# Kernel tuning notes

Measured on AMD Instinct MI355X. Metric: run time of the kernel, lower is better.

## Reference

```python
import jax, jax.numpy as jnp
import numpy as np

N_NODES = 100000

def gcn_conv(x, W, b, row, col, n):
    # PyG GCNConv: linear transform, then D^-1/2 A_hat D^-1/2 aggregation (+bias).
    xw = x @ W                                            # [N, out]
    deg = jax.ops.segment_sum(jnp.ones_like(col, dtype=xw.dtype), col, num_segments=n)
    dinv = jnp.where(deg > 0, jax.lax.rsqrt(jnp.maximum(deg, 1e-12)), 0.0)
    norm = dinv[row] * dinv[col]                          # [E]
    msgs = xw[row] * norm[:, None]                        # gather + scale
    out = jax.ops.segment_sum(msgs, col, num_segments=n)  # scatter-add
    return out + b


def setup_inputs() -> dict:
    key = jax.random.key(0)
    k = jax.random.split(key, 9)
    n, e = N_NODES, 1600000
    d_in, d_h, d_out = 128, 64, 40
    def glorot(kk, fi, fo):
        s = jnp.sqrt(6.0 / (fi + fo))
        return jax.random.uniform(kk, (fi, fo), jnp.float32, -s, s)
    return {
        "x": jax.random.normal(k[0], (n, d_in), jnp.float32),
        "edge_index": jax.random.randint(k[1], (2, e), 0, n, jnp.int64),
        "W1": glorot(k[2], d_in, d_h), "b1": jnp.zeros((d_h,), jnp.float32),
        "W2": glorot(k[3], d_h, d_h),  "b2": jnp.zeros((d_h,), jnp.float32),
        "W3": glorot(k[4], d_h, d_out), "b3": jnp.zeros((d_out,), jnp.float32),
    }


def reference(x, edge_index, W1, b1, W2, b2, W3, b3):
    n = x.shape[0]
    loops = jnp.arange(n, dtype=edge_index.dtype)
    row = jnp.concatenate([edge_index[0], loops])  # self-loops added, as in GCNConv
    col = jnp.concatenate([edge_index[1], loops])
    h = jax.nn.relu(gcn_conv(x, W1, b1, row, col, n))
    h = jax.nn.relu(gcn_conv(h, W2, b2, row, col, n))
    return gcn_conv(h, W3, b3, row, col, n)
```

## Files before the change

kernel.cpp:

```cpp
#include <hip/hip_runtime.h>
#include <hip/hip_fp16.h>

constexpr int TPB = 256;
constexpr int SH = 9;
constexpr int BD = 1 << SH;
constexpr int CHUNK = 4096;

typedef _Float16 half8 __attribute__((ext_vector_type(8)));
typedef float float4v __attribute__((ext_vector_type(4)));

__device__ __forceinline__ int wave_incl_scan(int x, int lane) {
#pragma unroll
  for (int d = 1; d < 64; d <<= 1) {
    int y = __shfl_up(x, d);
    if (lane >= d) x += y;
  }
  return x;
}


__global__ void bin_kernel(const int* __restrict__ row, const int* __restrict__ col,
                           int* __restrict__ bcur, int2* __restrict__ binned,
                           int e, int nb, int cap) {
  __shared__ int h[512];
  __shared__ int base[512];
  for (int i = threadIdx.x; i < nb; i += TPB) h[i] = 0;
  __syncthreads();
  int cb = blockIdx.x * CHUNK;
  int lim = min(cb + CHUNK, e);
  for (int i = cb + threadIdx.x; i < lim; i += TPB)
    atomicAdd(&h[col[i] >> SH], 1);
  __syncthreads();
  for (int i = threadIdx.x; i < nb; i += TPB) {
    int c = h[i];
    base[i] = c ? (i * cap + atomicAdd(&bcur[i], c)) : 0;
    h[i] = 0;
  }
  __syncthreads();
  for (int i = cb + threadIdx.x; i < lim; i += TPB) {
    int c = col[i];
    int b = c >> SH;
    int p = base[b] + atomicAdd(&h[b], 1);
    binned[p] = make_int2(row[i], c);
  }
}

__global__ __launch_bounds__(512) void count_place_kernel(
    const int2* __restrict__ binned, const int* __restrict__ bcnt, int cap,
    int2* __restrict__ offs2, float* __restrict__ dinv, int* __restrict__ csr, int n) {
  __shared__ int cnt[BD];
  __shared__ int wsum[8];
  int t = threadIdx.x, lane = t & 63, wv = t >> 6;
  int b = blockIdx.x;
  int c0 = b << SH;
  int ndst = min(BD, n - c0);
  cnt[t] = 0;
  __syncthreads();
  int beg = b * cap;
  int end = beg + bcnt[b];
  for (int i = beg + t; i < end; i += 512)
    atomicAdd(&cnt[binned[i].y - c0], 1);
  __syncthreads();
  int v = cnt[t];
  int ps = wave_incl_scan(v, lane);
  if (lane == 63) wsum[wv] = ps;
  __syncthreads();
  int woff = 0;
#pragma unroll
  for (int w = 0; w < 8; w++) woff += (w < wv) ? wsum[w] : 0;
  int ex = woff + ps - v;
  if (t < ndst) {
    offs2[c0 + t] = make_int2(beg + ex, beg + ex + v);
    dinv[c0 + t] = rsqrtf(1.0f + (float)v);
  }
  __syncthreads();
  cnt[t] = beg + ex;
  __syncthreads();
  for (int i = beg + t; i < end; i += 512) {
    int2 rc = binned[i];
    int p = atomicAdd(&cnt[rc.y - c0], 1);
    csr[p] = rc.x;
  }
}


template <int K, int M, int CT, int KT>
__device__ __forceinline__ void pack_one(const float* __restrict__ W,
                                         _Float16* __restrict__ P, int idx) {
  if (idx >= CT * KT * 64 * 8) return;
  int j = idx & 7;
  int lane = (idx >> 3) & 63;
  int f = idx >> 9;
  int kt = f % KT, ct = f / KT;
  int c = ct * 16 + (lane & 15);
  int k = kt * 32 + (lane >> 4) * 8 + j;
  float v = (c < M) ? W[k * M + c] : 0.f;
  P[idx] = (_Float16)v;
}

__global__ __launch_bounds__(256) void pack_all_kernel(
    const float* __restrict__ W1, const float* __restrict__ W2,
    const float* __restrict__ W3, _Float16* __restrict__ P1,
    _Float16* __restrict__ P2, _Float16* __restrict__ P3, int* __restrict__ bcur) {
  int blk = blockIdx.x, t = threadIdx.x;
  if (blk < 32) {
    pack_one<128, 64, 4, 4>(W1, P1, blk * 256 + t);
  } else if (blk < 48) {
    pack_one<64, 64, 4, 2>(W2, P2, (blk - 32) * 256 + t);
  } else if (blk < 60) {
    pack_one<64, 40, 3, 2>(W3, P3, (blk - 48) * 256 + t);
  } else {
    bcur[t] = 0;
    bcur[t + 256] = 0;
  }
}


template <int K, int M, int CT>
__global__ __launch_bounds__(256) void gemm_mfma_f32in(const float* __restrict__ x,
                                                       const _Float16* __restrict__ PW,
                                                       const float* __restrict__ dinv,
                                                       _Float16* __restrict__ out, int n) {
  constexpr int KT = K / 32;
  int lane = threadIdx.x & 63, wv = threadIdx.x >> 6;
  int m = lane & 15, q = lane >> 4;
  int row0w = blockIdx.x * 64 + wv * 16;
  int arow = row0w + m;
  int ar = arow < n ? arow : n - 1;
  const half8* pw = (const half8*)PW;

  float4v acc[CT];
#pragma unroll
  for (int ct = 0; ct < CT; ct++) acc[ct] = (float4v){0.f, 0.f, 0.f, 0.f};

#pragma unroll
  for (int kt = 0; kt < KT; kt++) {
    const float* xp = x + (size_t)ar * K + kt * 32 + q * 8;
    float4 x0 = *(const float4*)xp;
    float4 x1 = *(const float4*)(xp + 4);
    half8 a;
    a[0] = (_Float16)x0.x; a[1] = (_Float16)x0.y;
    a[2] = (_Float16)x0.z; a[3] = (_Float16)x0.w;
    a[4] = (_Float16)x1.x; a[5] = (_Float16)x1.y;
    a[6] = (_Float16)x1.z; a[7] = (_Float16)x1.w;
#pragma unroll
    for (int ct = 0; ct < CT; ct++) {
      half8 b = pw[(ct * KT + kt) * 64 + lane];
      acc[ct] = __builtin_amdgcn_mfma_f32_16x16x32_f16(a, b, acc[ct], 0, 0, 0);
    }
  }
  int r0 = row0w + q * 4;
  float dv[4];
#pragma unroll
  for (int reg = 0; reg < 4; reg++) dv[reg] = (r0 + reg < n) ? dinv[r0 + reg] : 0.f;
#pragma unroll
  for (int ct = 0; ct < CT; ct++) {
    int c = ct * 16 + m;
    if (c < M) {
#pragma unroll
      for (int reg = 0; reg < 4; reg++) {
        int r = r0 + reg;
        if (r < n) out[(size_t)r * M + c] = (_Float16)(acc[ct][reg] * dv[reg]);
      }
    }
  }
}

template <int K, int M, int CT>
__global__ __launch_bounds__(256) void gemm_mfma_f16in(const _Float16* __restrict__ x,
                                                       const _Float16* __restrict__ PW,
                                                       const float* __restrict__ dinv,
                                                       _Float16* __restrict__ out, int n) {
  constexpr int KT = K / 32;
  int lane = threadIdx.x & 63, wv = threadIdx.x >> 6;
  int m = lane & 15, q = lane >> 4;
  int row0w = blockIdx.x * 64 + wv * 16;
  int arow = row0w + m;
  int ar = arow < n ? arow : n - 1;
  const half8* pw = (const half8*)PW;

  float4v acc[CT];
#pragma unroll
  for (int ct = 0; ct < CT; ct++) acc[ct] = (float4v){0.f, 0.f, 0.f, 0.f};

#pragma unroll
  for (int kt = 0; kt < KT; kt++) {
    half8 a = *(const half8*)(x + (size_t)ar * K + kt * 32 + q * 8);
#pragma unroll
    for (int ct = 0; ct < CT; ct++) {
      half8 b = pw[(ct * KT + kt) * 64 + lane];
      acc[ct] = __builtin_amdgcn_mfma_f32_16x16x32_f16(a, b, acc[ct], 0, 0, 0);
    }
  }
  int r0 = row0w + q * 4;
  float dv[4];
#pragma unroll
  for (int reg = 0; reg < 4; reg++) dv[reg] = (r0 + reg < n) ? dinv[r0 + reg] : 0.f;
#pragma unroll
  for (int ct = 0; ct < CT; ct++) {
    int c = ct * 16 + m;
    if (c < M) {
#pragma unroll
      for (int reg = 0; reg < 4; reg++) {
        int r = r0 + reg;
        if (r < n) out[(size_t)r * M + c] = (_Float16)(acc[ct][reg] * dv[reg]);
      }
    }
  }
}

template <int K, int M, int CT>
__global__ __launch_bounds__(256) void gemm_mfma_f16in_f32out(
    const _Float16* __restrict__ x, const _Float16* __restrict__ PW,
    const float* __restrict__ bias, float* __restrict__ out, int n) {
  constexpr int KT = K / 32;
  int lane = threadIdx.x & 63, wv = threadIdx.x >> 6;
  int m = lane & 15, q = lane >> 4;
  int row0w = blockIdx.x * 64 + wv * 16;
  int arow = row0w + m;
  int ar = arow < n ? arow : n - 1;
  const half8* pw = (const half8*)PW;

  float4v acc[CT];
#pragma unroll
  for (int ct = 0; ct < CT; ct++) acc[ct] = (float4v){0.f, 0.f, 0.f, 0.f};

#pragma unroll
  for (int kt = 0; kt < KT; kt++) {
    half8 a = *(const half8*)(x + (size_t)ar * K + kt * 32 + q * 8);
#pragma unroll
    for (int ct = 0; ct < CT; ct++) {
      half8 b = pw[(ct * KT + kt) * 64 + lane];
      acc[ct] = __builtin_amdgcn_mfma_f32_16x16x32_f16(a, b, acc[ct], 0, 0, 0);
    }
  }
  int r0 = row0w + q * 4;
#pragma unroll
  for (int ct = 0; ct < CT; ct++) {
    int c = ct * 16 + m;
    if (c < M) {
      float bb = bias[c];
#pragma unroll
      for (int reg = 0; reg < 4; reg++) {
        int r = r0 + reg;
        if (r < n) out[(size_t)r * M + c] = acc[ct][reg] + bb;
      }
    }
  }
}


__device__ __forceinline__ void h8_add(uint4 u, float* acc) {
  __half2 h0 = *(__half2*)&u.x, h1 = *(__half2*)&u.y;
  __half2 h2 = *(__half2*)&u.z, h3 = *(__half2*)&u.w;
  float2 f0 = __half22float2(h0), f1 = __half22float2(h1);
  float2 f2 = __half22float2(h2), f3 = __half22float2(h3);
  acc[0] += f0.x; acc[1] += f0.y; acc[2] += f1.x; acc[3] += f1.y;
  acc[4] += f2.x; acc[5] += f2.y; acc[6] += f3.x; acc[7] += f3.y;
}

template <int MODE>
__global__ __launch_bounds__(256) void agg_kernel(
    const uint4* __restrict__ xw4, const float* __restrict__ dinv,
    const int* __restrict__ csr, const int2* __restrict__ offs2,
    const float* __restrict__ bias, uint4* __restrict__ out4, int n) {
  int lane = threadIdx.x & 63, wv = threadIdx.x >> 6;
  int slot = lane >> 3, fl = lane & 7;
  int sb = slot << 3;
  int i = blockIdx.x * 32 + wv * 8 + slot;
  bool valid = i < n;
  int ic = valid ? i : n - 1;
  int2 oe = offs2[ic];
  int beg = oe.x;
  int end = valid ? oe.y : beg;
  float di = dinv[ic];
  float acc[8] = {0.f, 0.f, 0.f, 0.f, 0.f, 0.f, 0.f, 0.f};
  h8_add(xw4[(size_t)ic * 8 + fl], acc);

  for (int b = beg; b < end; b += 8) {
    int idx = b + fl;
    int rr = 0;
    if (idx < end) rr = csr[idx];
    int cnt = end - b;
    uint4 u[8];
#pragma unroll
    for (int j = 0; j < 8; j++) {
      if (j < cnt) {
        int r = __shfl(rr, sb + j);
        u[j] = xw4[(size_t)r * 8 + fl];
      }
    }
#pragma unroll
    for (int j = 0; j < 8; j++) {
      if (j < cnt) h8_add(u[j], acc);
    }
  }

  if (valid) {
    float o[8];
    if (MODE < 2) {
      const float4* b4 = (const float4*)bias;
      float4 ba = b4[fl * 2], bb = b4[fl * 2 + 1];
      o[0] = fmaxf(acc[0] * di + ba.x, 0.f);
      o[1] = fmaxf(acc[1] * di + ba.y, 0.f);
      o[2] = fmaxf(acc[2] * di + ba.z, 0.f);
      o[3] = fmaxf(acc[3] * di + ba.w, 0.f);
      o[4] = fmaxf(acc[4] * di + bb.x, 0.f);
      o[5] = fmaxf(acc[5] * di + bb.y, 0.f);
      o[6] = fmaxf(acc[6] * di + bb.z, 0.f);
      o[7] = fmaxf(acc[7] * di + bb.w, 0.f);
      if (MODE == 1) {
#pragma unroll
        for (int k = 0; k < 8; k++) o[k] *= di;
      }
    } else {
#pragma unroll
      for (int k = 0; k < 8; k++) o[k] = acc[k] * di;
    }
    __half2 h0 = __float22half2_rn(make_float2(o[0], o[1]));
    __half2 h1 = __float22half2_rn(make_float2(o[2], o[3]));
    __half2 h2 = __float22half2_rn(make_float2(o[4], o[5]));
    __half2 h3 = __float22half2_rn(make_float2(o[6], o[7]));
    uint4 u;
    u.x = *(unsigned*)&h0;
    u.y = *(unsigned*)&h1;
    u.z = *(unsigned*)&h2;
    u.w = *(unsigned*)&h3;
    out4[(size_t)i * 8 + fl] = u;
  }
}


extern "C" void kernel_launch(void* const* d_in, const int* in_sizes, int n_in,
                              void* d_out, int out_size, void* d_ws, size_t ws_size,
                              hipStream_t stream) {
  const float* x  = (const float*)d_in[0];
  const int*   ei = (const int*)d_in[1];
  const float* W1 = (const float*)d_in[2];
  const float* b1 = (const float*)d_in[3];
  const float* W2 = (const float*)d_in[4];
  const float* b2 = (const float*)d_in[5];
  const float* W3 = (const float*)d_in[6];
  const float* b3 = (const float*)d_in[7];

  int n = in_sizes[0] / 128;
  int e = in_sizes[1] / 2;
  const int* rowA = ei;
  const int* colA = ei + e;

  int nb = (n + BD - 1) >> SH;
  int meanb = e / nb;
  int cap = meanb + (meanb / 4 > 1024 ? meanb / 4 : 1024);
  int nch = (e + CHUNK - 1) / CHUNK;

  size_t off = 0;
  auto alloc = [&](size_t bytes) {
    void* p = (char*)d_ws + off;
    off += (bytes + 255) & ~(size_t)255;
    return p;
  };
  __half* bufA  = (__half*)alloc((size_t)n * 64 * 4);
  __half* bufB  = (__half*)alloc((size_t)n * 64 * 4);
  int2*  offs2  = (int2*)alloc((size_t)n * 8);
  float* dinv   = (float*)alloc((size_t)n * 4);
  int*   csr    = (int*)alloc((size_t)nb * cap * 4);
  int*   bcur   = (int*)alloc(512 * 4);
  _Float16* PW1 = (_Float16*)alloc(4 * 4 * 64 * 8 * 2);
  _Float16* PW2 = (_Float16*)alloc(4 * 2 * 64 * 8 * 2);
  _Float16* PW3 = (_Float16*)alloc(3 * 2 * 64 * 8 * 2);
  int2*  binned = (int2*)bufA;
  (void)ws_size; (void)n_in; (void)out_size;

  pack_all_kernel<<<61, TPB, 0, stream>>>(W1, W2, W3, PW1, PW2, PW3, bcur);
  bin_kernel<<<nch, TPB, 0, stream>>>(rowA, colA, bcur, binned, e, nb, cap);
  count_place_kernel<<<nb, 512, 0, stream>>>(binned, bcur, cap, offs2, dinv, csr, n);

  int gmf = (n + 63) / 64;
  int gagg = (n + 31) / 32;
  gemm_mfma_f32in<128, 64, 4><<<gmf, TPB, 0, stream>>>(x, PW1, dinv, (_Float16*)bufA, n);
  agg_kernel<0><<<gagg, TPB, 0, stream>>>((const uint4*)bufA, dinv, csr, offs2,
                                          b1, (uint4*)bufB, n);
  gemm_mfma_f16in<64, 64, 4><<<gmf, TPB, 0, stream>>>((const _Float16*)bufB, PW2, dinv,
                                                      (_Float16*)bufA, n);
  agg_kernel<1><<<gagg, TPB, 0, stream>>>((const uint4*)bufA, dinv, csr, offs2,
                                          b2, (uint4*)bufB, n);
  agg_kernel<2><<<gagg, TPB, 0, stream>>>((const uint4*)bufB, dinv, csr, offs2,
                                          nullptr, (uint4*)bufA, n);
  gemm_mfma_f16in_f32out<64, 40, 3><<<gmf, TPB, 0, stream>>>((const _Float16*)bufA, PW3,
                                                             b3, (float*)d_out, n);
}
```

Measured before the change: 281.2 us.

## Fuse aggregation with following GEMM via LDS tile and widen per-node lanes

The first and third aggregations are merged with the GEMM that follows them. Each block aggregates 64 nodes into an fp16 LDS tile, then runs MFMA on that tile, which avoids writing the intermediate activations to global memory and reading them back. Aggregation now gives each node 16 lanes: two halves split the neighbours and are combined with a shuffle, and the next batch of CSR indices is prefetched. The cost is fewer nodes in flight per wave in the fused kernels (a serial loop over 4 nodes per slot), which may hurt latency hiding on the gather.

Result: faster. 256.5 us (-8.8%).

```diff
diff --git a/kernel.cpp b/kernel.cpp
--- a/kernel.cpp
+++ b/kernel.cpp
@@ -166,89 +166,6 @@
   }
 }
 
-template <int K, int M, int CT>
-__global__ __launch_bounds__(256) void gemm_mfma_f16in(const _Float16* __restrict__ x,
-                                                       const _Float16* __restrict__ PW,
-                                                       const float* __restrict__ dinv,
-                                                       _Float16* __restrict__ out, int n) {
-  constexpr int KT = K / 32;
-  int lane = threadIdx.x & 63, wv = threadIdx.x >> 6;
-  int m = lane & 15, q = lane >> 4;
-  int row0w = blockIdx.x * 64 + wv * 16;
-  int arow = row0w + m;
-  int ar = arow < n ? arow : n - 1;
-  const half8* pw = (const half8*)PW;
-
-  float4v acc[CT];
-#pragma unroll
-  for (int ct = 0; ct < CT; ct++) acc[ct] = (float4v){0.f, 0.f, 0.f, 0.f};
-
-#pragma unroll
-  for (int kt = 0; kt < KT; kt++) {
-    half8 a = *(const half8*)(x + (size_t)ar * K + kt * 32 + q * 8);
-#pragma unroll
-    for (int ct = 0; ct < CT; ct++) {
-      half8 b = pw[(ct * KT + kt) * 64 + lane];
-      acc[ct] = __builtin_amdgcn_mfma_f32_16x16x32_f16(a, b, acc[ct], 0, 0, 0);
-    }
-  }
-  int r0 = row0w + q * 4;
-  float dv[4];
-#pragma unroll
-  for (int reg = 0; reg < 4; reg++) dv[reg] = (r0 + reg < n) ? dinv[r0 + reg] : 0.f;
-#pragma unroll
-  for (int ct = 0; ct < CT; ct++) {
-    int c = ct * 16 + m;
-    if (c < M) {
-#pragma unroll
-      for (int reg = 0; reg < 4; reg++) {
-        int r = r0 + reg;
-        if (r < n) out[(size_t)r * M + c] = (_Float16)(acc[ct][reg] * dv[reg]);
-      }
-    }
-  }
-}
-
-template <int K, int M, int CT>
-__global__ __launch_bounds__(256) void gemm_mfma_f16in_f32out(
-    const _Float16* __restrict__ x, const _Float16* __restrict__ PW,
-    const float* __restrict__ bias, float* __restrict__ out, int n) {
-  constexpr int KT = K / 32;
-  int lane = threadIdx.x & 63, wv = threadIdx.x >> 6;
-  int m = lane & 15, q = lane >> 4;
-  int row0w = blockIdx.x * 64 + wv * 16;
-  int arow = row0w + m;
-  int ar = arow < n ? arow : n - 1;
-  const half8* pw = (const half8*)PW;
-
-  float4v acc[CT];
-#pragma unroll
-  for (int ct = 0; ct < CT; ct++) acc[ct] = (float4v){0.f, 0.f, 0.f, 0.f};
-
-#pragma unroll
-  for (int kt = 0; kt < KT; kt++) {
-    half8 a = *(const half8*)(x + (size_t)ar * K + kt * 32 + q * 8);
-#pragma unroll
-    for (int ct = 0; ct < CT; ct++) {
-      half8 b = pw[(ct * KT + kt) * 64 + lane];
-      acc[ct] = __builtin_amdgcn_mfma_f32_16x16x32_f16(a, b, acc[ct], 0, 0, 0);
-    }
-  }
-  int r0 = row0w + q * 4;
-#pragma unroll
-  for (int ct = 0; ct < CT; ct++) {
-    int c = ct * 16 + m;
-    if (c < M) {
-      float bb = bias[c];
-#pragma unroll
-      for (int reg = 0; reg < 4; reg++) {
-        int r = r0 + reg;
-        if (r < n) out[(size_t)r * M + c] = acc[ct][reg] + bb;
-      }
-    }
-  }
-}
-
 
 __device__ __forceinline__ void h8_add(uint4 u, float* acc) {
   __half2 h0 = *(__half2*)&u.x, h1 = *(__half2*)&u.y;
@@ -259,15 +176,62 @@
   acc[4] += f2.x; acc[5] += f2.y; acc[6] += f3.x; acc[7] += f3.y;
 }
 
-template <int MODE>
-__global__ __launch_bounds__(256) void agg_kernel(
+__device__ __forceinline__ uint4 pack_h8(const float* o) {
+  __half2 h0 = __float22half2_rn(make_float2(o[0], o[1]));
+  __half2 h1 = __float22half2_rn(make_float2(o[2], o[3]));
+  __half2 h2 = __float22half2_rn(make_float2(o[4], o[5]));
+  __half2 h3 = __float22half2_rn(make_float2(o[6], o[7]));
+  uint4 u;
+  u.x = *(unsigned*)&h0;
+  u.y = *(unsigned*)&h1;
+  u.z = *(unsigned*)&h2;
+  u.w = *(unsigned*)&h3;
+  return u;
+}
+
+__device__ __forceinline__ void agg_node(const uint4* __restrict__ xw4,
+                                         const int* __restrict__ csr,
+                                         int beg, int end, int sb, int half,
+                                         int fl, int fl16, float* acc) {
+  int b = beg;
+  int idx0 = b + fl16;
+  int rr = (idx0 < end) ? csr[idx0] : 0;
+  while (b < end) {
+    int bn = b + 16;
+    int idxn = bn + fl16;
+    int rn = (idxn < end) ? csr[idxn] : 0;
+    int cnt = end - b;
+    uint4 u[8];
+    int r[8];
+#pragma unroll
+    for (int j = 0; j < 8; j++) {
+      int ej = 2 * j + half;
+      r[j] = __shfl(rr, sb + ej);
+    }
+#pragma unroll
+    for (int j = 0; j < 8; j++) {
+      int ej = 2 * j + half;
+      if (ej < cnt) u[j] = xw4[(size_t)r[j] * 8 + fl];
+    }
+#pragma unroll
+    for (int j = 0; j < 8; j++) {
+      int ej = 2 * j + half;
+      if (ej < cnt) h8_add(u[j], acc);
+    }
+    rr = rn;
+    b = bn;
+  }
+}
+
+
+__global__ __launch_bounds__(256) void agg_mid_kernel(
     const uint4* __restrict__ xw4, const float* __restrict__ dinv,
     const int* __restrict__ csr, const int2* __restrict__ offs2,
     const float* __restrict__ bias, uint4* __restrict__ out4, int n) {
   int lane = threadIdx.x & 63, wv = threadIdx.x >> 6;
-  int slot = lane >> 3, fl = lane & 7;
-  int sb = slot << 3;
-  int i = blockIdx.x * 32 + wv * 8 + slot;
+  int sl = lane >> 4, fl16 = lane & 15, half = fl16 >> 3, fl = fl16 & 7;
+  int sb = sl << 4;
+  int i = blockIdx.x * 16 + wv * 4 + sl;
   bool valid = i < n;
   int ic = valid ? i : n - 1;
   int2 oe = offs2[ic];
@@ -275,31 +239,61 @@
   int end = valid ? oe.y : beg;
   float di = dinv[ic];
   float acc[8] = {0.f, 0.f, 0.f, 0.f, 0.f, 0.f, 0.f, 0.f};
-  h8_add(xw4[(size_t)ic * 8 + fl], acc);
-
-  for (int b = beg; b < end; b += 8) {
-    int idx = b + fl;
-    int rr = 0;
-    if (idx < end) rr = csr[idx];
-    int cnt = end - b;
-    uint4 u[8];
-#pragma unroll
-    for (int j = 0; j < 8; j++) {
-      if (j < cnt) {
-        int r = __shfl(rr, sb + j);
-        u[j] = xw4[(size_t)r * 8 + fl];
-      }
-    }
-#pragma unroll
-    for (int j = 0; j < 8; j++) {
-      if (j < cnt) h8_add(u[j], acc);
-    }
-  }
-
-  if (valid) {
+  if (!half) h8_add(xw4[(size_t)ic * 8 + fl], acc);
+  agg_node(xw4, csr, beg, end, sb, half, fl, fl16, acc);
+#pragma unroll
+  for (int k = 0; k < 8; k++) acc[k] += __shfl_xor(acc[k], 8);
+
+  if (valid && !half) {
+    const float4* b4 = (const float4*)bias;
+    float4 ba = b4[fl * 2], bb = b4[fl * 2 + 1];
     float o[8];
-    if (MODE < 2) {
-      const float4* b4 = (const float4*)bias;
+    o[0] = fmaxf(acc[0] * di + ba.x, 0.f) * di;
+    o[1] = fmaxf(acc[1] * di + ba.y, 0.f) * di;
+    o[2] = fmaxf(acc[2] * di + ba.z, 0.f) * di;
+    o[3] = fmaxf(acc[3] * di + ba.w, 0.f) * di;
+    o[4] = fmaxf(acc[4] * di + bb.x, 0.f) * di;
+    o[5] = fmaxf(acc[5] * di + bb.y, 0.f) * di;
+    o[6] = fmaxf(acc[6] * di + bb.z, 0.f) * di;
+    o[7] = fmaxf(acc[7] * di + bb.w, 0.f) * di;
+    out4[(size_t)i * 8 + fl] = pack_h8(o);
+  }
+}
+
+
+template <int M, int CT, int FMODE>
+__global__ __launch_bounds__(256) void fused_agg_gemm(
+    const uint4* __restrict__ xw4, const float* __restrict__ dinv,
+    const int* __restrict__ csr, const int2* __restrict__ offs2,
+    const float* __restrict__ biasA, const float* __restrict__ biasG,
+    const _Float16* __restrict__ PW, void* __restrict__ outp, int n) {
+  constexpr int KT = 2;
+  __shared__ _Float16 tile[64 * 72];
+  int lane = threadIdx.x & 63, wv = threadIdx.x >> 6;
+  int sl = lane >> 4, fl16 = lane & 15, half = fl16 >> 3, fl = fl16 & 7;
+  int sb = sl << 4;
+  int slot_id = wv * 4 + sl;
+  int base = blockIdx.x * 64;
+
+#pragma unroll 1
+  for (int nd = 0; nd < 4; nd++) {
+    int l = slot_id * 4 + nd;
+    int i = base + l;
+    bool valid = i < n;
+    int ic = valid ? i : n - 1;
+    int2 oe = offs2[ic];
+    int beg = oe.x;
+    int end = valid ? oe.y : beg;
+    float di = dinv[ic];
+    float acc[8] = {0.f, 0.f, 0.f, 0.f, 0.f, 0.f, 0.f, 0.f};
+    if (!half) h8_add(xw4[(size_t)ic * 8 + fl], acc);
+    agg_node(xw4, csr, beg, end, sb, half, fl, fl16, acc);
+#pragma unroll
+    for (int k = 0; k < 8; k++) acc[k] += __shfl_xor(acc[k], 8);
+
+    float o[8];
+    if (FMODE == 0) {
+      const float4* b4 = (const float4*)biasA;
       float4 ba = b4[fl * 2], bb = b4[fl * 2 + 1];
       o[0] = fmaxf(acc[0] * di + ba.x, 0.f);
       o[1] = fmaxf(acc[1] * di + ba.y, 0.f);
@@ -309,24 +303,60 @@
       o[5] = fmaxf(acc[5] * di + bb.y, 0.f);
       o[6] = fmaxf(acc[6] * di + bb.z, 0.f);
       o[7] = fmaxf(acc[7] * di + bb.w, 0.f);
-      if (MODE == 1) {
-#pragma unroll
-        for (int k = 0; k < 8; k++) o[k] *= di;
+    } else {
+#pragma unroll
+      for (int k = 0; k < 8; k++) o[k] = acc[k] * di;
+    }
+    if (!half) *(uint4*)&tile[(size_t)l * 72 + fl * 8] = pack_h8(o);
+  }
+  __syncthreads();
+
+  int m = lane & 15, q = lane >> 4;
+  int lrow = wv * 16 + m;
+  const half8* pw = (const half8*)PW;
+  float4v accd[CT];
+#pragma unroll
+  for (int ct = 0; ct < CT; ct++) accd[ct] = (float4v){0.f, 0.f, 0.f, 0.f};
+#pragma unroll
+  for (int kt = 0; kt < KT; kt++) {
+    half8 a = *(const half8*)&tile[lrow * 72 + kt * 32 + q * 8];
+#pragma unroll
+    for (int ct = 0; ct < CT; ct++) {
+      half8 b = pw[(ct * KT + kt) * 64 + lane];
+      accd[ct] = __builtin_amdgcn_mfma_f32_16x16x32_f16(a, b, accd[ct], 0, 0, 0);
+    }
+  }
+  int r0 = base + wv * 16 + q * 4;
+  if (FMODE == 0) {
+    _Float16* out = (_Float16*)outp;
+    float dv[4];
+#pragma unroll
+    for (int reg = 0; reg < 4; reg++) dv[reg] = (r0 + reg < n) ? dinv[r0 + reg] : 0.f;
+#pragma unroll
+    for (int ct = 0; ct < CT; ct++) {
+      int c = ct * 16 + m;
+      if (c < M) {
+#pragma unroll
+        for (int reg = 0; reg < 4; reg++) {
+          int r = r0 + reg;
+          if (r < n) out[(size_t)r * M + c] = (_Float16)(accd[ct][reg] * dv[reg]);
+        }
       }
-    } else {
-#pragma unroll
-      for (int k = 0; k < 8; k++) o[k] = acc[k] * di;
-    }
-    __half2 h0 = __float22half2_rn(make_float2(o[0], o[1]));
-    __half2 h1 = __float22half2_rn(make_float2(o[2], o[3]));
-    __half2 h2 = __float22half2_rn(make_float2(o[4], o[5]));
-    __half2 h3 = __float22half2_rn(make_float2(o[6], o[7]));
-    uint4 u;
-    u.x = *(unsigned*)&h0;
-    u.y = *(unsigned*)&h1;
-    u.z = *(unsigned*)&h2;
-    u.w = *(unsigned*)&h3;
-    out4[(size_t)i * 8 + fl] = u;
+    }
+  } else {
+    float* out = (float*)outp;
+#pragma unroll
+    for (int ct = 0; ct < CT; ct++) {
+      int c = ct * 16 + m;
+      if (c < M) {
+        float bb = biasG[c];
+#pragma unroll
+        for (int reg = 0; reg < 4; reg++) {
+          int r = r0 + reg;
+          if (r < n) out[(size_t)r * M + c] = accd[ct][reg] + bb;
+        }
+      }
+    }
   }
 }
 
@@ -376,16 +406,13 @@
   count_place_kernel<<<nb, 512, 0, stream>>>(binned, bcur, cap, offs2, dinv, csr, n);
 
   int gmf = (n + 63) / 64;
-  int gagg = (n + 31) / 32;
+  int gagg = (n + 15) / 16;
+
   gemm_mfma_f32in<128, 64, 4><<<gmf, TPB, 0, stream>>>(x, PW1, dinv, (_Float16*)bufA, n);
-  agg_kernel<0><<<gagg, TPB, 0, stream>>>((const uint4*)bufA, dinv, csr, offs2,
-                                          b1, (uint4*)bufB, n);
-  gemm_mfma_f16in<64, 64, 4><<<gmf, TPB, 0, stream>>>((const _Float16*)bufB, PW2, dinv,
-                                                      (_Float16*)bufA, n);
-  agg_kernel<1><<<gagg, TPB, 0, stream>>>((const uint4*)bufA, dinv, csr, offs2,
-                                          b2, (uint4*)bufB, n);
-  agg_kernel<2><<<gagg, TPB, 0, stream>>>((const uint4*)bufB, dinv, csr, offs2,
-                                          nullptr, (uint4*)bufA, n);
-  gemm_mfma_f16in_f32out<64, 40, 3><<<gmf, TPB, 0, stream>>>((const _Float16*)bufA, PW3,
-                                                             b3, (float*)d_out, n);
-}
+  fused_agg_gemm<64, 4, 0><<<gmf, TPB, 0, stream>>>(
+      (const uint4*)bufA, dinv, csr, offs2, b1, nullptr, PW2, bufB, n);
+  agg_mid_kernel<<<gagg, TPB, 0, stream>>>((const uint4*)bufB, dinv, csr, offs2,
+                                           b2, (uint4*)bufA, n);
+  fused_agg_gemm<40, 3, 1><<<gmf, TPB, 0, stream>>>(
+      (const uint4*)bufA, dinv, csr, offs2, nullptr, b3, PW3, d_out, n);
+}
```

## Pack binned edges into 32-bit words and prefetch CSR indices in aggregation

Applied to the files above, without the earlier changes.

Binning now packs the local destination offset (9 bits) and the source row (23 bits) into a single int, which halves the binned-edge traffic in bin and count_place. The aggregation kernel drops the shuffle-based index broadcast. Each 8-lane group now loads 16 neighbor indices directly per iteration and prefetches the next 16 while it gathers features, aiming for more memory-level parallelism. The costs are a 2^23 node limit on row ids and more registers. Every lane also reads the same csr entries redundantly.

Result: slower. 312.2 us (+11.1%).

```diff
diff --git a/kernel.cpp b/kernel.cpp
--- a/kernel.cpp
+++ b/kernel.cpp
@@ -5,6 +5,7 @@
 constexpr int SH = 9;
 constexpr int BD = 1 << SH;
 constexpr int CHUNK = 4096;
+constexpr int RMASK = (1 << 23) - 1;
 
 typedef _Float16 half8 __attribute__((ext_vector_type(8)));
 typedef float float4v __attribute__((ext_vector_type(4)));
@@ -20,7 +21,7 @@
 
 
 __global__ void bin_kernel(const int* __restrict__ row, const int* __restrict__ col,
-                           int* __restrict__ bcur, int2* __restrict__ binned,
+                           int* __restrict__ bcur, int* __restrict__ binned,
                            int e, int nb, int cap) {
   __shared__ int h[512];
   __shared__ int base[512];
@@ -41,12 +42,12 @@
     int c = col[i];
     int b = c >> SH;
     int p = base[b] + atomicAdd(&h[b], 1);
-    binned[p] = make_int2(row[i], c);
+    binned[p] = ((c & (BD - 1)) << 23) | row[i];
   }
 }
 
 __global__ __launch_bounds__(512) void count_place_kernel(
-    const int2* __restrict__ binned, const int* __restrict__ bcnt, int cap,
+    const int* __restrict__ binned, const int* __restrict__ bcnt, int cap,
     int2* __restrict__ offs2, float* __restrict__ dinv, int* __restrict__ csr, int n) {
   __shared__ int cnt[BD];
   __shared__ int wsum[8];
@@ -59,7 +60,7 @@
   int beg = b * cap;
   int end = beg + bcnt[b];
   for (int i = beg + t; i < end; i += 512)
-    atomicAdd(&cnt[binned[i].y - c0], 1);
+    atomicAdd(&cnt[(unsigned)binned[i] >> 23], 1);
   __syncthreads();
   int v = cnt[t];
   int ps = wave_incl_scan(v, lane);
@@ -77,9 +78,9 @@
   cnt[t] = beg + ex;
   __syncthreads();
   for (int i = beg + t; i < end; i += 512) {
-    int2 rc = binned[i];
-    int p = atomicAdd(&cnt[rc.y - c0], 1);
-    csr[p] = rc.x;
+    int pv = binned[i];
+    int p = atomicAdd(&cnt[(unsigned)pv >> 23], 1);
+    csr[p] = pv;
   }
 }
 
@@ -166,6 +167,7 @@
   }
 }
 
+
 template <int K, int M, int CT>
 __global__ __launch_bounds__(256) void gemm_mfma_f16in(const _Float16* __restrict__ x,
                                                        const _Float16* __restrict__ PW,
@@ -209,6 +211,7 @@
   }
 }
 
+
 template <int K, int M, int CT>
 __global__ __launch_bounds__(256) void gemm_mfma_f16in_f32out(
     const _Float16* __restrict__ x, const _Float16* __restrict__ PW,
@@ -250,84 +253,96 @@
 }
 
 
-__device__ __forceinline__ void h8_add(uint4 u, float* acc) {
+__device__ __forceinline__ void h8_unpack(uint4 u, float* f) {
   __half2 h0 = *(__half2*)&u.x, h1 = *(__half2*)&u.y;
   __half2 h2 = *(__half2*)&u.z, h3 = *(__half2*)&u.w;
   float2 f0 = __half22float2(h0), f1 = __half22float2(h1);
   float2 f2 = __half22float2(h2), f3 = __half22float2(h3);
-  acc[0] += f0.x; acc[1] += f0.y; acc[2] += f1.x; acc[3] += f1.y;
-  acc[4] += f2.x; acc[5] += f2.y; acc[6] += f3.x; acc[7] += f3.y;
+  f[0] = f0.x; f[1] = f0.y; f[2] = f1.x; f[3] = f1.y;
+  f[4] = f2.x; f[5] = f2.y; f[6] = f3.x; f[7] = f3.y;
+}
+
+__device__ __forceinline__ uint4 pack_h8v(const float* o) {
+  __half2 h0 = __float22half2_rn(make_float2(o[0], o[1]));
+  __half2 h1 = __float22half2_rn(make_float2(o[2], o[3]));
+  __half2 h2 = __float22half2_rn(make_float2(o[4], o[5]));
+  __half2 h3 = __float22half2_rn(make_float2(o[6], o[7]));
+  uint4 u;
+  u.x = *(unsigned*)&h0;
+  u.y = *(unsigned*)&h1;
+  u.z = *(unsigned*)&h2;
+  u.w = *(unsigned*)&h3;
+  return u;
 }
 
 template <int MODE>
-__global__ __launch_bounds__(256) void agg_kernel(
+__global__ __launch_bounds__(256) void agg_dest_kernel(
     const uint4* __restrict__ xw4, const float* __restrict__ dinv,
     const int* __restrict__ csr, const int2* __restrict__ offs2,
     const float* __restrict__ bias, uint4* __restrict__ out4, int n) {
-  int lane = threadIdx.x & 63, wv = threadIdx.x >> 6;
-  int slot = lane >> 3, fl = lane & 7;
-  int sb = slot << 3;
-  int i = blockIdx.x * 32 + wv * 8 + slot;
-  bool valid = i < n;
-  int ic = valid ? i : n - 1;
-  int2 oe = offs2[ic];
-  int beg = oe.x;
-  int end = valid ? oe.y : beg;
-  float di = dinv[ic];
+  int t = threadIdx.x;
+  int g = t >> 3, fl = t & 7;
+  int i = blockIdx.x * 32 + g;
+  if (i >= n) return;
+  int2 oe = offs2[i];
+  int beg = oe.x, end = oe.y;
   float acc[8] = {0.f, 0.f, 0.f, 0.f, 0.f, 0.f, 0.f, 0.f};
-  h8_add(xw4[(size_t)ic * 8 + fl], acc);
-
-  for (int b = beg; b < end; b += 8) {
-    int idx = b + fl;
-    int rr = 0;
-    if (idx < end) rr = csr[idx];
+
+  int r[16];
+#pragma unroll
+  for (int j = 0; j < 16; j++) {
+    int idx = beg + j;
+    r[j] = (idx < end) ? (csr[idx] & RMASK) : 0;
+  }
+#pragma unroll 1
+  for (int b = beg; b < end; b += 16) {
     int cnt = end - b;
-    uint4 u[8];
-#pragma unroll
-    for (int j = 0; j < 8; j++) {
+    uint4 u[16];
+#pragma unroll
+    for (int j = 0; j < 16; j++)
+      if (j < cnt) u[j] = xw4[(size_t)r[j] * 8 + fl];
+    int bn = b + 16;
+#pragma unroll
+    for (int j = 0; j < 16; j++) {
+      int idx = bn + j;
+      r[j] = (idx < end) ? (csr[idx] & RMASK) : 0;
+    }
+#pragma unroll
+    for (int j = 0; j < 16; j++) {
       if (j < cnt) {
-        int r = __shfl(rr, sb + j);
-        u[j] = xw4[(size_t)r * 8 + fl];
+        float f[8];
+        h8_unpack(u[j], f);
+#pragma unroll
+        for (int k = 0; k < 8; k++) acc[k] += f[k];
       }
     }
-#pragma unroll
-    for (int j = 0; j < 8; j++) {
-      if (j < cnt) h8_add(u[j], acc);
-    }
-  }
-
-  if (valid) {
-    float o[8];
-    if (MODE < 2) {
-      const float4* b4 = (const float4*)bias;
-      float4 ba = b4[fl * 2], bb = b4[fl * 2 + 1];
-      o[0] = fmaxf(acc[0] * di + ba.x, 0.f);
-      o[1] = fmaxf(acc[1] * di + ba.y, 0.f);
-      o[2] = fmaxf(acc[2] * di + ba.z, 0.f);
-      o[3] = fmaxf(acc[3] * di + ba.w, 0.f);
-      o[4] = fmaxf(acc[4] * di + bb.x, 0.f);
-      o[5] = fmaxf(acc[5] * di + bb.y, 0.f);
-      o[6] = fmaxf(acc[6] * di + bb.z, 0.f);
-      o[7] = fmaxf(acc[7] * di + bb.w, 0.f);
-      if (MODE == 1) {
-#pragma unroll
-        for (int k = 0; k < 8; k++) o[k] *= di;
-      }
-    } else {
-#pragma unroll
-      for (int k = 0; k < 8; k++) o[k] = acc[k] * di;
-    }
-    __half2 h0 = __float22half2_rn(make_float2(o[0], o[1]));
-    __half2 h1 = __float22half2_rn(make_float2(o[2], o[3]));
-    __half2 h2 = __float22half2_rn(make_float2(o[4], o[5]));
-    __half2 h3 = __float22half2_rn(make_float2(o[6], o[7]));
-    uint4 u;
-    u.x = *(unsigned*)&h0;
-    u.y = *(unsigned*)&h1;
-    u.z = *(unsigned*)&h2;
-    u.w = *(unsigned*)&h3;
-    out4[(size_t)i * 8 + fl] = u;
-  }
+  }
+
+  uint4 sv = xw4[(size_t)i * 8 + fl];
+  float sf[8];
+  h8_unpack(sv, sf);
+  float di = dinv[i];
+  float o[8];
+  if (MODE < 2) {
+    const float4* b4 = (const float4*)bias;
+    float4 ba = b4[fl * 2], bb = b4[fl * 2 + 1];
+    o[0] = fmaxf((acc[0] + sf[0]) * di + ba.x, 0.f);
+    o[1] = fmaxf((acc[1] + sf[1]) * di + ba.y, 0.f);
+    o[2] = fmaxf((acc[2] + sf[2]) * di + ba.z, 0.f);
+    o[3] = fmaxf((acc[3] + sf[3]) * di + ba.w, 0.f);
+    o[4] = fmaxf((acc[4] + sf[4]) * di + bb.x, 0.f);
+    o[5] = fmaxf((acc[5] + sf[5]) * di + bb.y, 0.f);
+    o[6] = fmaxf((acc[6] + sf[6]) * di + bb.z, 0.f);
+    o[7] = fmaxf((acc[7] + sf[7]) * di + bb.w, 0.f);
+    if (MODE == 1) {
+#pragma unroll
+      for (int k = 0; k < 8; k++) o[k] *= di;
+    }
+  } else {
+#pragma unroll
+    for (int k = 0; k < 8; k++) o[k] = (acc[k] + sf[k]) * di;
+  }
+  out4[(size_t)i * 8 + fl] = pack_h8v(o);
 }
 
 
@@ -359,8 +374,9 @@
     off += (bytes + 255) & ~(size_t)255;
     return p;
   };
-  __half* bufA  = (__half*)alloc((size_t)n * 64 * 4);
-  __half* bufB  = (__half*)alloc((size_t)n * 64 * 4);
+  __half* bufA  = (__half*)alloc((size_t)n * 64 * 2);
+  __half* bufB  = (__half*)alloc((size_t)n * 64 * 2);
+  __half* bufC  = (__half*)alloc((size_t)n * 64 * 2);
   int2*  offs2  = (int2*)alloc((size_t)n * 8);
   float* dinv   = (float*)alloc((size_t)n * 4);
   int*   csr    = (int*)alloc((size_t)nb * cap * 4);
@@ -368,7 +384,7 @@
   _Float16* PW1 = (_Float16*)alloc(4 * 4 * 64 * 8 * 2);
   _Float16* PW2 = (_Float16*)alloc(4 * 2 * 64 * 8 * 2);
   _Float16* PW3 = (_Float16*)alloc(3 * 2 * 64 * 8 * 2);
-  int2*  binned = (int2*)bufA;
+  int*   binned = (int*)bufA;
   (void)ws_size; (void)n_in; (void)out_size;
 
   pack_all_kernel<<<61, TPB, 0, stream>>>(W1, W2, W3, PW1, PW2, PW3, bcur);
@@ -377,15 +393,16 @@
 
   int gmf = (n + 63) / 64;
   int gagg = (n + 31) / 32;
+
   gemm_mfma_f32in<128, 64, 4><<<gmf, TPB, 0, stream>>>(x, PW1, dinv, (_Float16*)bufA, n);
-  agg_kernel<0><<<gagg, TPB, 0, stream>>>((const uint4*)bufA, dinv, csr, offs2,
-                                          b1, (uint4*)bufB, n);
+  agg_dest_kernel<0><<<gagg, TPB, 0, stream>>>((const uint4*)bufA, dinv, csr, offs2,
+                                               b1, (uint4*)bufB, n);
   gemm_mfma_f16in<64, 64, 4><<<gmf, TPB, 0, stream>>>((const _Float16*)bufB, PW2, dinv,
-                                                      (_Float16*)bufA, n);
-  agg_kernel<1><<<gagg, TPB, 0, stream>>>((const uint4*)bufA, dinv, csr, offs2,
-                                          b2, (uint4*)bufB, n);
-  agg_kernel<2><<<gagg, TPB, 0, stream>>>((const uint4*)bufB, dinv, csr, offs2,
-                                          nullptr, (uint4*)bufA, n);
-  gemm_mfma_f16in_f32out<64, 40, 3><<<gmf, TPB, 0, stream>>>((const _Float16*)bufA, PW3,
+                                                      (_Float16*)bufC, n);
+  agg_dest_kernel<1><<<gagg, TPB, 0, stream>>>((const uint4*)bufC, dinv, csr, offs2,
+                                               b2, (uint4*)bufA, n);
+  agg_dest_kernel<2><<<gagg, TPB, 0, stream>>>((const uint4*)bufA, dinv, csr, offs2,
+                                               nullptr, (uint4*)bufB, n);
+  gemm_mfma_f16in_f32out<64, 40, 3><<<gmf, TPB, 0, stream>>>((const _Float16*)bufB, PW3,
                                                              b3, (float*)d_out, n);
 }
```
